# Performance work log

Measured on AMD Instinct MI355X. Metric: run time of the kernel, lower is better.

Reference implementation:

```python
import jax, jax.numpy as jnp
import numpy as np

TAU = 0.25    # membrane decay
GAMA = 1.0    # surrogate-gradient width

@jax.custom_vjp
def zif(u):
    # Heaviside spike with rectangular surrogate gradient (ZIF)
    return (u > 0).astype(u.dtype)

def _zif_fwd(u):
    return zif(u), u

def _zif_bwd(u, g):
    tmp = (1.0 / (GAMA * GAMA)) * jnp.clip(GAMA - jnp.abs(u), 0.0)
    return (g * tmp,)

zif.defvjp(_zif_fwd, _zif_bwd)


def setup_inputs() -> dict:
    key = jax.random.key(0)
    k1, _ = jax.random.split(key)
    x = jax.random.normal(k1, (32, 16, 65536), dtype=jnp.float32)  # [B, T, N]
    thresh = jnp.ones((1,), dtype=jnp.float32)                     # learnable threshold
    return {"x": x, "thresh": thresh}


def reference(x, thresh):
    # x: [B, T, N]; sequential LIF recurrence over T via lax.scan
    xT = jnp.moveaxis(x, 1, 0)  # [T, B, N]

    def step(mem, xt):
        mem = mem * TAU + xt                 # decay + integrate
        spike = zif(mem - thresh)            # threshold spike
        mem = (1.0 - spike) * mem            # multiplicative reset
        return mem, spike

    mem0 = jnp.zeros_like(xT[0])
    _, spikes = jax.lax.scan(step, mem0, xT)  # spikes: [T, B, N]
    return jnp.moveaxis(spikes, 0, 1)         # [B, T, N]
```

## Files before the change

### kernel.cpp

```cpp
#include <hip/hip_runtime.h>


#define TAU 0.25f

__global__ __launch_bounds__(256) void lif_fwd_kernel(
    const float4* __restrict__ x,
    const float* __restrict__ thresh,
    float4* __restrict__ out)
{
    constexpr int T  = 16;
    constexpr int N4 = 65536 / 4;

    const int gid = blockIdx.x * blockDim.x + threadIdx.x;
    const int b   = gid >> 14;
    const int n4  = gid & (N4 - 1);

    const float th = thresh[0];

    const size_t base = (size_t)b * T * N4 + n4;
    const float4* xp = x   + base;
    float4*       op = out + base;

    float4 mem = make_float4(0.f, 0.f, 0.f, 0.f);

#pragma unroll
    for (int t = 0; t < T; ++t) {
        float4 xt = xp[(size_t)t * N4];

        mem.x = mem.x * TAU + xt.x;
        mem.y = mem.y * TAU + xt.y;
        mem.z = mem.z * TAU + xt.z;
        mem.w = mem.w * TAU + xt.w;

        const bool px = mem.x > th;
        const bool py = mem.y > th;
        const bool pz = mem.z > th;
        const bool pw = mem.w > th;

        float4 s;
        s.x = px ? 1.f : 0.f;
        s.y = py ? 1.f : 0.f;
        s.z = pz ? 1.f : 0.f;
        s.w = pw ? 1.f : 0.f;

        mem.x = px ? 0.f : mem.x;
        mem.y = py ? 0.f : mem.y;
        mem.z = pz ? 0.f : mem.z;
        mem.w = pw ? 0.f : mem.w;

        op[(size_t)t * N4] = s;
    }
}

extern "C" void kernel_launch(void* const* d_in, const int* in_sizes, int n_in,
                              void* d_out, int out_size, void* d_ws, size_t ws_size,
                              hipStream_t stream)
{
    const float* x      = (const float*)d_in[0];
    const float* thresh = (const float*)d_in[1];
    float*       out    = (float*)d_out;

    const int total   = in_sizes[0];
    const int threads = total / (16 * 4);
    const int block   = 256;
    const int grid    = threads / block;

    lif_fwd_kernel<<<grid, block, 0, stream>>>(
        (const float4*)x, thresh, (float4*)out);
}
```

Baseline: 234.7 us.

## Use float2 per thread, preload all timesteps, and nontemporal stores

Each thread now handles two neurons instead of four, which doubles the thread count. All 16 timestep loads are issued up front, before the recurrence runs, so more memory requests are in flight at once. Output spikes are written with nontemporal stores so they do not pollute the cache. The cost is narrower 8-byte accesses per thread and more registers held for the preloaded inputs.

New measurement: 228.5 us. 1.03x faster.

```diff
diff --git a/kernel.cpp b/kernel.cpp
--- a/kernel.cpp
+++ b/kernel.cpp
@@ -3,52 +3,49 @@
 
 #define TAU 0.25f
 
+typedef float f32x2 __attribute__((ext_vector_type(2)));
+
 __global__ __launch_bounds__(256) void lif_fwd_kernel(
-    const float4* __restrict__ x,
+    const f32x2* __restrict__ x,
     const float* __restrict__ thresh,
-    float4* __restrict__ out)
+    f32x2* __restrict__ out)
 {
     constexpr int T  = 16;
-    constexpr int N4 = 65536 / 4;
+    constexpr int N2 = 65536 / 2;
 
     const int gid = blockIdx.x * blockDim.x + threadIdx.x;
-    const int b   = gid >> 14;
-    const int n4  = gid & (N4 - 1);
+    const int b   = gid >> 15;
+    const int n2  = gid & (N2 - 1);
 
     const float th = thresh[0];
 
-    const size_t base = (size_t)b * T * N4 + n4;
-    const float4* xp = x   + base;
-    float4*       op = out + base;
+    const size_t base = (size_t)b * T * N2 + n2;
+    const f32x2* xp = x   + base;
+    f32x2*       op = out + base;
 
-    float4 mem = make_float4(0.f, 0.f, 0.f, 0.f);
+    f32x2 xt[T];
+#pragma unroll
+    for (int t = 0; t < T; ++t)
+        xt[t] = xp[(size_t)t * N2];
+
+    f32x2 mem = {0.f, 0.f};
 
 #pragma unroll
     for (int t = 0; t < T; ++t) {
-        float4 xt = xp[(size_t)t * N4];
-
-        mem.x = mem.x * TAU + xt.x;
-        mem.y = mem.y * TAU + xt.y;
-        mem.z = mem.z * TAU + xt.z;
-        mem.w = mem.w * TAU + xt.w;
+        mem.x = mem.x * TAU + xt[t].x;
+        mem.y = mem.y * TAU + xt[t].y;
 
         const bool px = mem.x > th;
         const bool py = mem.y > th;
-        const bool pz = mem.z > th;
-        const bool pw = mem.w > th;
 
-        float4 s;
+        f32x2 s;
         s.x = px ? 1.f : 0.f;
         s.y = py ? 1.f : 0.f;
-        s.z = pz ? 1.f : 0.f;
-        s.w = pw ? 1.f : 0.f;
 
         mem.x = px ? 0.f : mem.x;
         mem.y = py ? 0.f : mem.y;
-        mem.z = pz ? 0.f : mem.z;
-        mem.w = pw ? 0.f : mem.w;
 
-        op[(size_t)t * N4] = s;
+        __builtin_nontemporal_store(s, &op[(size_t)t * N2]);
     }
 }
 
@@ -61,10 +58,10 @@
     float*       out    = (float*)d_out;
 
     const int total   = in_sizes[0];
-    const int threads = total / (16 * 4);
+    const int threads = total / (16 * 2);
     const int block   = 256;
     const int grid    = threads / block;
 
     lif_fwd_kernel<<<grid, block, 0, stream>>>(
-        (const float4*)x, thresh, (float4*)out);
+        (const f32x2*)x, thresh, (f32x2*)out);
 }
```

## Stage inputs into LDS via direct global-to-LDS loads, nontemporal stores

Applied to the files above, without the earlier changes.

Each block now fetches all 16 timesteps of a 1024-element tile with global_load_lds DMA into shared memory before computing, so all loads are in flight at once instead of being serialized by the recurrence. Output uses nontemporal stores to avoid polluting cache. It uses 64KB of LDS per block, which limits occupancy, and the full wait before compute removes any load/compute overlap within a block.

Measured after the change: 231.2 us. No clear change (-1.5%).

```diff
diff --git a/kernel.cpp b/kernel.cpp
--- a/kernel.cpp
+++ b/kernel.cpp
@@ -3,29 +3,49 @@
 
 #define TAU 0.25f
 
+typedef float f32x4 __attribute__((ext_vector_type(4)));
+
 __global__ __launch_bounds__(256) void lif_fwd_kernel(
-    const float4* __restrict__ x,
+    const float* __restrict__ x,
     const float* __restrict__ thresh,
-    float4* __restrict__ out)
+    float* __restrict__ out)
 {
-    constexpr int T  = 16;
-    constexpr int N4 = 65536 / 4;
+    constexpr int T    = 16;
+    constexpr int N    = 65536;
+    constexpr int TILE = 1024;
 
-    const int gid = blockIdx.x * blockDim.x + threadIdx.x;
-    const int b   = gid >> 14;
-    const int n4  = gid & (N4 - 1);
+    __shared__ float lds[T * TILE];
 
-    const float th = thresh[0];
+    const int tid  = threadIdx.x;
+    const int wave = tid >> 6;
+    const int lane = tid & 63;
 
-    const size_t base = (size_t)b * T * N4 + n4;
-    const float4* xp = x   + base;
-    float4*       op = out + base;
+    const int tile_idx = blockIdx.x & 63;
+    const int b        = blockIdx.x >> 6;
 
-    float4 mem = make_float4(0.f, 0.f, 0.f, 0.f);
+    const size_t row0 = (size_t)b * T * N + (size_t)tile_idx * TILE;
 
 #pragma unroll
     for (int t = 0; t < T; ++t) {
-        float4 xt = xp[(size_t)t * N4];
+        const float* gsrc = x + row0 + (size_t)t * N + wave * 256 + lane * 4;
+        float*       ldst = lds + t * TILE + wave * 256;
+        __builtin_amdgcn_global_load_lds(
+            (const __attribute__((address_space(1))) void*)gsrc,
+            (__attribute__((address_space(3))) void*)ldst,
+            16, 0, 0);
+    }
+
+    asm volatile("s_waitcnt vmcnt(0)" ::: "memory");
+    __builtin_amdgcn_sched_barrier(0);
+
+    const float th  = thresh[0];
+    const int   col = tid * 4;
+
+    f32x4 mem = {0.f, 0.f, 0.f, 0.f};
+
+#pragma unroll
+    for (int t = 0; t < T; ++t) {
+        f32x4 xt = *(const f32x4*)(lds + t * TILE + col);
 
         mem.x = mem.x * TAU + xt.x;
         mem.y = mem.y * TAU + xt.y;
@@ -37,7 +57,7 @@
         const bool pz = mem.z > th;
         const bool pw = mem.w > th;
 
-        float4 s;
+        f32x4 s;
         s.x = px ? 1.f : 0.f;
         s.y = py ? 1.f : 0.f;
         s.z = pz ? 1.f : 0.f;
@@ -48,7 +68,7 @@
         mem.z = pz ? 0.f : mem.z;
         mem.w = pw ? 0.f : mem.w;
 
-        op[(size_t)t * N4] = s;
+        __builtin_nontemporal_store(s, (f32x4*)(out + row0 + (size_t)t * N + col));
     }
 }
 
@@ -60,11 +80,9 @@
     const float* thresh = (const float*)d_in[1];
     float*       out    = (float*)d_out;
 
-    const int total   = in_sizes[0];
-    const int threads = total / (16 * 4);
-    const int block   = 256;
-    const int grid    = threads / block;
+    const int total = in_sizes[0];
+    const int grid  = total / (16 * 1024);
+    const int block = 256;
 
-    lif_fwd_kernel<<<grid, block, 0, stream>>>(
-        (const float4*)x, thresh, (float4*)out);
+    lif_fwd_kernel<<<grid, block, 0, stream>>>(x, thresh, out);
 }
```
